# Kernel optimization log

Measured on AMD Instinct MI355X. Metric: run time of the kernel, lower is better.

## Reference

```python
import jax, jax.numpy as jnp
import numpy as np

N = 100000      # nodes
E = 1600000     # edges (avg degree 16)
IN_DIM = 64
OUT_DIM = 128
BN_EPS = 1e-5


def setup_inputs() -> dict:
    key = jax.random.key(0)
    kx, ke, kw, kb, ks = jax.random.split(key, 5)
    x = jax.random.normal(kx, (N, IN_DIM), dtype=jnp.float32)
    edge_index = jax.random.randint(ke, (2, E), 0, N, dtype=jnp.int32)
    # GCNConv linear weight (no bias inside lin; conv bias separate)
    W = jax.random.normal(kw, (IN_DIM, OUT_DIM), dtype=jnp.float32) / np.sqrt(IN_DIM)
    bias = jax.random.normal(kb, (OUT_DIM,), dtype=jnp.float32) * 0.01
    # skip projection Linear(in_dim, out_dim, bias=False)
    skip_W = jax.random.normal(ks, (IN_DIM, OUT_DIM), dtype=jnp.float32) / np.sqrt(IN_DIM)
    # BatchNorm1d affine params (training-mode batch stats used in forward)
    gamma = jnp.ones((OUT_DIM,), dtype=jnp.float32)
    beta = jnp.zeros((OUT_DIM,), dtype=jnp.float32)
    return {"x": x, "edge_index": edge_index, "W": W, "bias": bias,
            "skip_W": skip_W, "gamma": gamma, "beta": beta}


def _gcn_forward(x, edge_index, W, bias, skip_W, gamma, beta):
    n = x.shape[0]
    # GCNConv, normalize=True, add_self_loops=True (PyG defaults)
    row, col = edge_index[0], edge_index[1]
    loop = jnp.arange(n, dtype=edge_index.dtype)
    row_f = jnp.concatenate([row, loop])   # source nodes
    col_f = jnp.concatenate([col, loop])   # target nodes

    xt = x @ W                             # [N, OUT]
    deg = jax.ops.segment_sum(jnp.ones_like(col_f, dtype=xt.dtype), col_f,
                              num_segments=n)          # >= 1 due to self loops
    dinv = jax.lax.rsqrt(deg)
    norm = dinv[row_f] * dinv[col_f]                    # [E+N]
    msgs = xt[row_f] * norm[:, None]                    # gather + scale
    out = jax.ops.segment_sum(msgs, col_f, num_segments=n) + bias

    # skip-sum (in_dim != out_dim -> project)
    out = out + x @ skip_W

    # BatchNorm1d (training-mode batch statistics), affine
    mean = out.mean(axis=0)
    var = out.var(axis=0)
    out = (out - mean) * jax.lax.rsqrt(var + BN_EPS) * gamma + beta

    # ReLU; dropout p=0.0 -> identity
    return jax.nn.relu(out)


def reference(x, edge_index, W, bias, skip_W, gamma, beta):
    return _gcn_forward(x, edge_index, W, bias, skip_W, gamma, beta)
```

## Files before the change

### kernel.cpp

```cpp
#include <hip/hip_runtime.h>


typedef unsigned short ushort;
typedef __bf16 bf16x8 __attribute__((ext_vector_type(8)));
typedef float f32x4 __attribute__((ext_vector_type(4)));
typedef float f32x2 __attribute__((ext_vector_type(2)));

constexpr int N_NODES = 100000;
constexpr int N_PAD   = 100096;
constexpr int E_EDGES = 1600000;

constexpr int BUCK_SHIFT = 7;
constexpr int NBUCK   = (N_NODES + 127) / 128;
constexpr int NBUCK_P = 784;
constexpr int CHUNK   = 4096;
constexpr int NCHUNK  = (E_EDGES + CHUNK - 1) / CHUNK;
constexpr int SORT_CAP = 4096;

constexpr size_t OFF_SCALE  = 0;
constexpr size_t OFF_DINV   = 256;
constexpr size_t OFF_ROWPTR = 100352;
constexpr size_t OFF_BASE   = 200480;
constexpr size_t OFF_GHIST  = 201280;
constexpr size_t OFF_PART   = OFF_GHIST;
constexpr size_t OFF_BINNED = 507824;
constexpr size_t OFF_XB     = 2107824;
constexpr size_t OFF_U      = 5310896;
constexpr size_t OFF_PRE    = 8513968;
constexpr size_t OFF_XD8    = OFF_PRE;
constexpr size_t OFF_BT     = 14920112;

static __device__ __forceinline__ ushort f2bf(float f) {
    union { float f; unsigned u; } v; v.f = f;
    unsigned r = v.u + 0x7FFFu + ((v.u >> 16) & 1u);
    return (ushort)(r >> 16);
}
static __device__ __forceinline__ float bf2f(ushort u) {
    union { unsigned u; float f; } v; v.u = (unsigned)u << 16;
    return v.f;
}
static __device__ __forceinline__ unsigned pack_fp8x4(float a, float b, float c, float d) {
    int r = 0;
    r = __builtin_amdgcn_cvt_pk_fp8_f32(a, b, r, false);
    r = __builtin_amdgcn_cvt_pk_fp8_f32(c, d, r, true);
    return (unsigned)r;
}

__global__ void k_prep(const float* __restrict__ W, const float* __restrict__ skipW,
                       ushort* __restrict__ Bt) {
    int t = blockIdx.x * 256 + threadIdx.x;
    if (t >= 128 * 128) return;
    int k = t >> 7, n = t & 127;
    float v = (k < 64) ? W[k * 128 + n] : skipW[(k - 64) * 128 + n];
    Bt[n * 128 + k] = f2bf(v);
}

__global__ __launch_bounds__(256) void k_hist(const int* __restrict__ col,
                                              int* __restrict__ gh) {
    __shared__ int h[NBUCK_P];
    int c = blockIdx.x, t = threadIdx.x;
    for (int b = t; b < NBUCK_P; b += 256) h[b] = 0;
    __syncthreads();
    int e0 = c * CHUNK;
#pragma unroll
    for (int i = 0; i < CHUNK / 256; ++i) {
        int e = e0 + i * 256 + t;
        if (e < E_EDGES) atomicAdd(&h[col[e] >> BUCK_SHIFT], 1);
    }
    __syncthreads();
    for (int b = t; b < NBUCK_P; b += 256) gh[c * NBUCK_P + b] = h[b];
}

__global__ __launch_bounds__(512) void k_scan_buckets(int* __restrict__ gh,
                                                      int* __restrict__ base) {
    __shared__ int lds[512];
    int b = blockIdx.x, t = threadIdx.x;
    int v = (t < NCHUNK) ? gh[t * NBUCK_P + b] : 0;
    lds[t] = v;
    __syncthreads();
    int val = v;
#pragma unroll
    for (int off = 1; off < 512; off <<= 1) {
        int add = (t >= off) ? lds[t - off] : 0;
        __syncthreads();
        val += add;
        lds[t] = val;
        __syncthreads();
    }
    if (t < NCHUNK) gh[t * NBUCK_P + b] = val - v;
    if (t == 511) base[b] = val;
}

__global__ __launch_bounds__(1024) void k_scan_bases(int* __restrict__ base,
                                                     int* __restrict__ rowptr) {
    __shared__ int lds[1024];
    int t = threadIdx.x;
    int v = (t < NBUCK) ? base[t] : 0;
    lds[t] = v;
    __syncthreads();
    int val = v;
#pragma unroll
    for (int off = 1; off < 1024; off <<= 1) {
        int add = (t >= off) ? lds[t - off] : 0;
        __syncthreads();
        val += add;
        lds[t] = val;
        __syncthreads();
    }
    if (t < NBUCK) base[t] = val - v;
    if (t == 1023) {
        base[NBUCK] = val;
        rowptr[N_NODES] = val;
    }
}

__global__ __launch_bounds__(256) void k_scatter_bin(const int* __restrict__ row,
                                                     const int* __restrict__ col,
                                                     const int* __restrict__ gh,
                                                     const int* __restrict__ base,
                                                     unsigned int* __restrict__ binned) {
    __shared__ int cur[NBUCK_P];
    int c = blockIdx.x, t = threadIdx.x;
    for (int b = t; b < NBUCK_P; b += 256) {
        int bb = (b < NBUCK) ? base[b] : 0;
        cur[b] = bb + gh[c * NBUCK_P + b];
    }
    __syncthreads();
    int e0 = c * CHUNK;
#pragma unroll
    for (int i = 0; i < CHUNK / 256; ++i) {
        int e = e0 + i * 256 + t;
        if (e < E_EDGES) {
            int d = col[e];
            int s = row[e];
            int p = atomicAdd(&cur[d >> BUCK_SHIFT], 1);
            binned[p] = ((unsigned int)(d & 127) << 17) | (unsigned int)s;
        }
    }
}

__global__ __launch_bounds__(256) void k_sortbucket(unsigned int* __restrict__ binned,
                                                    const int* __restrict__ base,
                                                    int* __restrict__ rowptr,
                                                    float* __restrict__ dinv,
                                                    const float* __restrict__ x,
                                                    ushort* __restrict__ xb,
                                                    unsigned* __restrict__ xd8) {
    __shared__ unsigned int ebuf[SORT_CAP];
    __shared__ int sbuf[SORT_CAP];
    __shared__ int lcnt[128];
    __shared__ int scanb[128];
    __shared__ int lptr[128];
    __shared__ float ldinv[128];
    int b = blockIdx.x, t = threadIdx.x;
    int i0 = base[b], i1 = base[b + 1];
    int cnt = i1 - i0;
    if (cnt > SORT_CAP) cnt = SORT_CAP;
    int n0 = b << BUCK_SHIFT;
    int nn = min(128, N_NODES - n0);

    for (int k = t; k < cnt; k += 256) ebuf[k] = binned[i0 + k];
    if (t < 128) lcnt[t] = 0;
    __syncthreads();
    for (int k = t; k < cnt; k += 256) atomicAdd(&lcnt[ebuf[k] >> 17], 1);
    __syncthreads();

    int myc = (t < 128) ? lcnt[t] : 0;
    if (t < 128) scanb[t] = myc;
    __syncthreads();
    int val = myc;
#pragma unroll
    for (int off = 1; off < 128; off <<= 1) {
        int add = (t < 128 && t >= off) ? scanb[t - off] : 0;
        __syncthreads();
        if (t < 128) {
            val += add;
            scanb[t] = val;
        }
        __syncthreads();
    }
    if (t < 128) {
        int excl = val - myc;
        lptr[t] = excl;
        float dv = rsqrtf((float)myc + 1.0f);
        ldinv[t] = dv;
        if (t < nn) {
            rowptr[n0 + t] = i0 + excl;
            dinv[n0 + t] = dv;
        }
    }
    __syncthreads();
    for (int k = t; k < cnt; k += 256) {
        unsigned int e = ebuf[k];
        int j = (int)(e >> 17);
        int p = atomicAdd(&lptr[j], 1);
        sbuf[p] = (int)(e & 0x1FFFF);
    }
    __syncthreads();
    for (int k = t; k < cnt; k += 256) binned[i0 + k] = (unsigned int)sbuf[k];

#pragma unroll
    for (int it = 0; it < 8; ++it) {
        int idx = it * 256 + t;
        int nl = idx >> 4, q = idx & 15;
        int c = n0 + nl;
        ushort4 bb = {0, 0, 0, 0};
        unsigned w8 = 0;
        if (nl < nn) {
            float4 v = ((const float4*)x)[(size_t)c * 16 + q];
            bb.x = f2bf(v.x); bb.y = f2bf(v.y); bb.z = f2bf(v.z); bb.w = f2bf(v.w);
            float d = ldinv[nl];
            w8 = pack_fp8x4(v.x * d, v.y * d, v.z * d, v.w * d);
        }
        ((ushort4*)xb)[(size_t)c * 16 + q] = bb;
        xd8[(size_t)c * 16 + q] = w8;
    }
}

__global__ __launch_bounds__(256) void k_agg(const unsigned* __restrict__ xd8,
                                             const float* __restrict__ dinv,
                                             const int* __restrict__ rowptr,
                                             const unsigned int* __restrict__ csr,
                                             ushort* __restrict__ u) {
    int t = blockIdx.x * blockDim.x + threadIdx.x;
    if (t >= N_PAD * 16) return;
    int c = t >> 4;
    int q = t & 15;
    if (c >= N_NODES) {
        ushort4 z = {0, 0, 0, 0};
        ((ushort4*)u)[t] = z;
        return;
    }
    float dc = dinv[c];
    float4 acc;
    {
        unsigned w = xd8[t];
        f32x2 lo = __builtin_amdgcn_cvt_pk_f32_fp8((int)w, false);
        f32x2 hi = __builtin_amdgcn_cvt_pk_f32_fp8((int)w, true);
        acc.x = lo.x; acc.y = lo.y; acc.z = hi.x; acc.w = hi.y;
    }
    int i0 = rowptr[c], i1 = rowptr[c + 1];
    int i = i0;
    for (; i + 8 <= i1; i += 8) {
        int s[8];
#pragma unroll
        for (int k = 0; k < 8; ++k) s[k] = (int)csr[i + k];
        unsigned w[8];
#pragma unroll
        for (int k = 0; k < 8; ++k) w[k] = xd8[s[k] * 16 + q];
#pragma unroll
        for (int k = 0; k < 8; ++k) {
            f32x2 lo = __builtin_amdgcn_cvt_pk_f32_fp8((int)w[k], false);
            f32x2 hi = __builtin_amdgcn_cvt_pk_f32_fp8((int)w[k], true);
            acc.x += lo.x; acc.y += lo.y; acc.z += hi.x; acc.w += hi.y;
        }
    }
    for (; i < i1; ++i) {
        unsigned w = xd8[(int)csr[i] * 16 + q];
        f32x2 lo = __builtin_amdgcn_cvt_pk_f32_fp8((int)w, false);
        f32x2 hi = __builtin_amdgcn_cvt_pk_f32_fp8((int)w, true);
        acc.x += lo.x; acc.y += lo.y; acc.z += hi.x; acc.w += hi.y;
    }
    ushort4 o;
    o.x = f2bf(acc.x * dc); o.y = f2bf(acc.y * dc);
    o.z = f2bf(acc.z * dc); o.w = f2bf(acc.w * dc);
    ((ushort4*)u)[t] = o;
}

__global__ __launch_bounds__(256) void k_gemm(const ushort* __restrict__ u,
                                              const ushort* __restrict__ xb,
                                              const ushort* __restrict__ Bt,
                                              const float* __restrict__ bias,
                                              ushort* __restrict__ pre,
                                              float* __restrict__ partial) {
    __shared__ float sred[128];
    __shared__ float qred[128];
    int tid = threadIdx.x;
    int wave = tid >> 6, lane = tid & 63;
    int wm = wave >> 1, wn = wave & 1;
    int l15 = lane & 15, quad = lane >> 4;
    int row0 = blockIdx.x * 128 + wm * 64;
    int col0 = wn * 64;

    if (tid < 128) { sred[tid] = 0.f; qred[tid] = 0.f; }
    __syncthreads();

    bf16x8 af[4][4], bf_[4][4];
#pragma unroll
    for (int kc = 0; kc < 4; ++kc) {
        const ushort* abase = (kc < 2) ? u : xb;
        int ko = (kc & 1) * 32 + quad * 8;
#pragma unroll
        for (int im = 0; im < 4; ++im)
            af[kc][im] = *(const bf16x8*)&abase[(size_t)(row0 + im * 16 + l15) * 64 + ko];
#pragma unroll
        for (int jn = 0; jn < 4; ++jn)
            bf_[kc][jn] = *(const bf16x8*)&Bt[(size_t)(col0 + jn * 16 + l15) * 128 + kc * 32 + quad * 8];
    }

    f32x4 acc[4][4];
#pragma unroll
    for (int a = 0; a < 4; ++a)
#pragma unroll
        for (int b = 0; b < 4; ++b) acc[a][b] = (f32x4){0.f, 0.f, 0.f, 0.f};

#pragma unroll
    for (int kc = 0; kc < 4; ++kc)
#pragma unroll
        for (int im = 0; im < 4; ++im)
#pragma unroll
            for (int jn = 0; jn < 4; ++jn)
                acc[im][jn] = __builtin_amdgcn_mfma_f32_16x16x32_bf16(
                    af[kc][im], bf_[kc][jn], acc[im][jn], 0, 0, 0);

    int coln[4];
    float bi[4];
#pragma unroll
    for (int jn = 0; jn < 4; ++jn) {
        coln[jn] = col0 + jn * 16 + l15;
        bi[jn] = bias[coln[jn]];
    }
    float lsum[4] = {0.f, 0.f, 0.f, 0.f};
    float lsq[4]  = {0.f, 0.f, 0.f, 0.f};
#pragma unroll
    for (int im = 0; im < 4; ++im) {
        int rbase = row0 + im * 16 + quad * 4;
#pragma unroll
        for (int r = 0; r < 4; ++r) {
            int rowi = rbase + r;
            if (rowi < N_NODES) {
#pragma unroll
                for (int jn = 0; jn < 4; ++jn) {
                    float v = acc[im][jn][r] + bi[jn];
                    pre[(size_t)rowi * 128 + coln[jn]] = f2bf(v);
                    lsum[jn] += v;
                    lsq[jn]  += v * v;
                }
            }
        }
    }
#pragma unroll
    for (int jn = 0; jn < 4; ++jn) {
        atomicAdd(&sred[coln[jn]], lsum[jn]);
        atomicAdd(&qred[coln[jn]], lsq[jn]);
    }
    __syncthreads();
    if (tid < 128) {
        partial[(size_t)blockIdx.x * 256 + tid]       = sred[tid];
        partial[(size_t)blockIdx.x * 256 + 128 + tid] = qred[tid];
    }
}

__global__ __launch_bounds__(256) void k_reduce(const float* __restrict__ partial,
                                                const float* __restrict__ gamma,
                                                const float* __restrict__ beta,
                                                float* __restrict__ scaleshift) {
    __shared__ float ls[256], lq[256];
    int j = blockIdx.x;
    int t = threadIdx.x;
    float s = 0.f, q = 0.f;
    for (int p = t; p < NBUCK; p += 256) {
        s += partial[(size_t)p * 256 + j];
        q += partial[(size_t)p * 256 + 128 + j];
    }
    ls[t] = s; lq[t] = q;
    __syncthreads();
#pragma unroll
    for (int off = 128; off > 0; off >>= 1) {
        if (t < off) { ls[t] += ls[t + off]; lq[t] += lq[t + off]; }
        __syncthreads();
    }
    if (t == 0) {
        float mean = ls[0] * (1.0f / N_NODES);
        float var  = lq[0] * (1.0f / N_NODES) - mean * mean;
        float sc   = gamma[j] * rsqrtf(var + 1e-5f);
        scaleshift[j]       = sc;
        scaleshift[128 + j] = beta[j] - mean * sc;
    }
}

__global__ void k_apply(const ushort* __restrict__ pre, float* __restrict__ out,
                        const float* __restrict__ scaleshift) {
    int t = blockIdx.x * blockDim.x + threadIdx.x;
    if (t >= N_NODES * 32) return;
    int j4 = t & 31;
    ushort4 p = ((const ushort4*)pre)[t];
    float4 sc = ((const float4*)scaleshift)[j4];
    float4 sh = ((const float4*)(scaleshift + 128))[j4];
    float4 v;
    v.x = fmaxf(fmaf(bf2f(p.x), sc.x, sh.x), 0.f);
    v.y = fmaxf(fmaf(bf2f(p.y), sc.y, sh.y), 0.f);
    v.z = fmaxf(fmaf(bf2f(p.z), sc.z, sh.z), 0.f);
    v.w = fmaxf(fmaf(bf2f(p.w), sc.w, sh.w), 0.f);
    ((float4*)out)[t] = v;
}

extern "C" void kernel_launch(void* const* d_in, const int* in_sizes, int n_in,
                              void* d_out, int out_size, void* d_ws, size_t ws_size,
                              hipStream_t stream) {
    const float* x      = (const float*)d_in[0];
    const int*   eidx   = (const int*)d_in[1];
    const float* W      = (const float*)d_in[2];
    const float* bias   = (const float*)d_in[3];
    const float* skipW  = (const float*)d_in[4];
    const float* gamma  = (const float*)d_in[5];
    const float* beta   = (const float*)d_in[6];
    float* out = (float*)d_out;
    float* ws  = (float*)d_ws;

    const int* row = eidx;
    const int* col = eidx + E_EDGES;

    float* scaleshift = ws + OFF_SCALE;
    float* dinv       = ws + OFF_DINV;
    int*   rowptr     = (int*)(ws + OFF_ROWPTR);
    int*   base       = (int*)(ws + OFF_BASE);
    int*   gh         = (int*)(ws + OFF_GHIST);
    float* partial    = ws + OFF_PART;
    unsigned int* binned = (unsigned int*)(ws + OFF_BINNED);
    ushort* xb        = (ushort*)(ws + OFF_XB);
    ushort* u         = (ushort*)(ws + OFF_U);
    unsigned* xd8     = (unsigned*)(ws + OFF_XD8);
    ushort* pre       = (ushort*)(ws + OFF_PRE);
    ushort* Bt        = (ushort*)(ws + OFF_BT);

    k_prep<<<64, 256, 0, stream>>>(W, skipW, Bt);
    k_hist<<<NCHUNK, 256, 0, stream>>>(col, gh);
    k_scan_buckets<<<NBUCK, 512, 0, stream>>>(gh, base);
    k_scan_bases<<<1, 1024, 0, stream>>>(base, rowptr);
    k_scatter_bin<<<NCHUNK, 256, 0, stream>>>(row, col, gh, base, binned);
    k_sortbucket<<<NBUCK, 256, 0, stream>>>(binned, base, rowptr, dinv, x, xb, xd8);
    k_agg<<<(N_PAD * 16 + 255) / 256, 256, 0, stream>>>(xd8, dinv, rowptr, binned, u);
    k_gemm<<<NBUCK, 256, 0, stream>>>(u, xb, Bt, bias, pre, partial);
    k_reduce<<<128, 256, 0, stream>>>(partial, gamma, beta, scaleshift);
    k_apply<<<(N_NODES * 32 + 255) / 256, 256, 0, stream>>>(pre, out, scaleshift);
}
```

Baseline: 230.0 us.

## Merge prep into hist, fuse base scan via last-block, vectorize edge loads

Folds the weight transpose/convert kernel into the histogram kernel as extra blocks. It also removes the separate single-block base-scan kernel by having the last-finishing bucket-scan block, detected with an atomic counter, do the final scan. Edge index loads in hist and scatter are vectorized to int4, and the per-bucket 128-entry scan uses wavefront shuffles instead of LDS barriers. The aim is fewer kernel launches and less sync overhead, at the cost of an extra memset and reliance on atomic release/acquire ordering.

```diff
diff --git a/kernel.cpp b/kernel.cpp
--- a/kernel.cpp
+++ b/kernel.cpp
@@ -21,6 +21,7 @@
 constexpr size_t OFF_DINV   = 256;
 constexpr size_t OFF_ROWPTR = 100352;
 constexpr size_t OFF_BASE   = 200480;
+constexpr size_t OFF_DONE   = 201272;
 constexpr size_t OFF_GHIST  = 201280;
 constexpr size_t OFF_PART   = OFF_GHIST;
 constexpr size_t OFF_BINNED = 507824;
@@ -46,34 +47,51 @@
     return (unsigned)r;
 }
 
-__global__ void k_prep(const float* __restrict__ W, const float* __restrict__ skipW,
-                       ushort* __restrict__ Bt) {
-    int t = blockIdx.x * 256 + threadIdx.x;
-    if (t >= 128 * 128) return;
-    int k = t >> 7, n = t & 127;
-    float v = (k < 64) ? W[k * 128 + n] : skipW[(k - 64) * 128 + n];
-    Bt[n * 128 + k] = f2bf(v);
-}
-
 __global__ __launch_bounds__(256) void k_hist(const int* __restrict__ col,
-                                              int* __restrict__ gh) {
+                                              int* __restrict__ gh,
+                                              const float* __restrict__ W,
+                                              const float* __restrict__ skipW,
+                                              ushort* __restrict__ Bt) {
+    int c = blockIdx.x, t = threadIdx.x;
+    if (c >= NCHUNK) {
+        int idx = (c - NCHUNK) * 256 + t;
+        int k = idx >> 7, n = idx & 127;
+        float v = (k < 64) ? W[k * 128 + n] : skipW[(k - 64) * 128 + n];
+        Bt[n * 128 + k] = f2bf(v);
+        return;
+    }
     __shared__ int h[NBUCK_P];
-    int c = blockIdx.x, t = threadIdx.x;
     for (int b = t; b < NBUCK_P; b += 256) h[b] = 0;
     __syncthreads();
-    int e0 = c * CHUNK;
-#pragma unroll
-    for (int i = 0; i < CHUNK / 256; ++i) {
-        int e = e0 + i * 256 + t;
-        if (e < E_EDGES) atomicAdd(&h[col[e] >> BUCK_SHIFT], 1);
+    const int4* col4 = (const int4*)col;
+    int g0 = c * (CHUNK / 4);
+#pragma unroll
+    for (int i = 0; i < CHUNK / 1024; ++i) {
+        int g4 = g0 + i * 256 + t;
+        if (g4 * 4 + 3 < E_EDGES) {
+            int4 cc = col4[g4];
+            atomicAdd(&h[cc.x >> BUCK_SHIFT], 1);
+            atomicAdd(&h[cc.y >> BUCK_SHIFT], 1);
+            atomicAdd(&h[cc.z >> BUCK_SHIFT], 1);
+            atomicAdd(&h[cc.w >> BUCK_SHIFT], 1);
+        } else {
+#pragma unroll
+            for (int j = 0; j < 4; ++j) {
+                int e = g4 * 4 + j;
+                if (e < E_EDGES) atomicAdd(&h[col[e] >> BUCK_SHIFT], 1);
+            }
+        }
     }
     __syncthreads();
     for (int b = t; b < NBUCK_P; b += 256) gh[c * NBUCK_P + b] = h[b];
 }
 
 __global__ __launch_bounds__(512) void k_scan_buckets(int* __restrict__ gh,
-                                                      int* __restrict__ base) {
-    __shared__ int lds[512];
+                                                      int* __restrict__ base,
+                                                      int* __restrict__ rowptr,
+                                                      int* __restrict__ done) {
+    __shared__ int lds[1024];
+    __shared__ int lastflag;
     int b = blockIdx.x, t = threadIdx.x;
     int v = (t < NCHUNK) ? gh[t * NBUCK_P + b] : 0;
     lds[t] = v;
@@ -88,29 +106,35 @@
         __syncthreads();
     }
     if (t < NCHUNK) gh[t * NBUCK_P + b] = val - v;
-    if (t == 511) base[b] = val;
-}
-
-__global__ __launch_bounds__(1024) void k_scan_bases(int* __restrict__ base,
-                                                     int* __restrict__ rowptr) {
-    __shared__ int lds[1024];
-    int t = threadIdx.x;
-    int v = (t < NBUCK) ? base[t] : 0;
-    lds[t] = v;
-    __syncthreads();
-    int val = v;
+    if (t == 511) {
+        __hip_atomic_store(&base[b], val, __ATOMIC_RELEASE, __HIP_MEMORY_SCOPE_AGENT);
+        int old = __hip_atomic_fetch_add(done, 1, __ATOMIC_ACQ_REL, __HIP_MEMORY_SCOPE_AGENT);
+        lastflag = (old == NBUCK - 1) ? 1 : 0;
+    }
+    __syncthreads();
+    if (!lastflag) return;
+
+    int v0 = (t < NBUCK) ? __hip_atomic_load(&base[t], __ATOMIC_ACQUIRE, __HIP_MEMORY_SCOPE_AGENT) : 0;
+    int v1 = (512 + t < NBUCK) ? __hip_atomic_load(&base[512 + t], __ATOMIC_ACQUIRE, __HIP_MEMORY_SCOPE_AGENT) : 0;
+    __syncthreads();
+    lds[t] = v0;
+    lds[512 + t] = v1;
+    __syncthreads();
 #pragma unroll
     for (int off = 1; off < 1024; off <<= 1) {
-        int add = (t >= off) ? lds[t - off] : 0;
+        int a0 = (t >= off) ? lds[t - off] : 0;
+        int a1 = (512 + t >= off) ? lds[512 + t - off] : 0;
         __syncthreads();
-        val += add;
-        lds[t] = val;
+        lds[t] += a0;
+        lds[512 + t] += a1;
         __syncthreads();
     }
-    if (t < NBUCK) base[t] = val - v;
-    if (t == 1023) {
-        base[NBUCK] = val;
-        rowptr[N_NODES] = val;
+    if (t < NBUCK) base[t] = lds[t] - v0;
+    if (512 + t < NBUCK) base[512 + t] = lds[512 + t] - v1;
+    if (t == 511) {
+        int total = lds[1023];
+        base[NBUCK] = total;
+        rowptr[N_NODES] = total;
     }
 }
 
@@ -126,15 +150,34 @@
         cur[b] = bb + gh[c * NBUCK_P + b];
     }
     __syncthreads();
-    int e0 = c * CHUNK;
-#pragma unroll
-    for (int i = 0; i < CHUNK / 256; ++i) {
-        int e = e0 + i * 256 + t;
-        if (e < E_EDGES) {
-            int d = col[e];
-            int s = row[e];
-            int p = atomicAdd(&cur[d >> BUCK_SHIFT], 1);
-            binned[p] = ((unsigned int)(d & 127) << 17) | (unsigned int)s;
+    const int4* col4 = (const int4*)col;
+    const int4* row4 = (const int4*)row;
+    int g0 = c * (CHUNK / 4);
+#pragma unroll
+    for (int i = 0; i < CHUNK / 1024; ++i) {
+        int g4 = g0 + i * 256 + t;
+        if (g4 * 4 + 3 < E_EDGES) {
+            int4 cc = col4[g4];
+            int4 rr = row4[g4];
+            int p;
+            p = atomicAdd(&cur[cc.x >> BUCK_SHIFT], 1);
+            binned[p] = ((unsigned)(cc.x & 127) << 17) | (unsigned)rr.x;
+            p = atomicAdd(&cur[cc.y >> BUCK_SHIFT], 1);
+            binned[p] = ((unsigned)(cc.y & 127) << 17) | (unsigned)rr.y;
+            p = atomicAdd(&cur[cc.z >> BUCK_SHIFT], 1);
+            binned[p] = ((unsigned)(cc.z & 127) << 17) | (unsigned)rr.z;
+            p = atomicAdd(&cur[cc.w >> BUCK_SHIFT], 1);
+            binned[p] = ((unsigned)(cc.w & 127) << 17) | (unsigned)rr.w;
+        } else {
+#pragma unroll
+            for (int j = 0; j < 4; ++j) {
+                int e = g4 * 4 + j;
+                if (e < E_EDGES) {
+                    int d = col[e], s = row[e];
+                    int p = atomicAdd(&cur[d >> BUCK_SHIFT], 1);
+                    binned[p] = ((unsigned)(d & 127) << 17) | (unsigned)s;
+                }
+            }
         }
     }
 }
@@ -149,9 +192,9 @@
     __shared__ unsigned int ebuf[SORT_CAP];
     __shared__ int sbuf[SORT_CAP];
     __shared__ int lcnt[128];
-    __shared__ int scanb[128];
     __shared__ int lptr[128];
     __shared__ float ldinv[128];
+    __shared__ int wsum[2];
     int b = blockIdx.x, t = threadIdx.x;
     int i0 = base[b], i1 = base[b + 1];
     int cnt = i1 - i0;
@@ -165,21 +208,20 @@
     for (int k = t; k < cnt; k += 256) atomicAdd(&lcnt[ebuf[k] >> 17], 1);
     __syncthreads();
 
-    int myc = (t < 128) ? lcnt[t] : 0;
-    if (t < 128) scanb[t] = myc;
-    __syncthreads();
-    int val = myc;
-#pragma unroll
-    for (int off = 1; off < 128; off <<= 1) {
-        int add = (t < 128 && t >= off) ? scanb[t - off] : 0;
-        __syncthreads();
-        if (t < 128) {
-            val += add;
-            scanb[t] = val;
-        }
-        __syncthreads();
-    }
+    int myc = 0, val = 0;
     if (t < 128) {
+        myc = lcnt[t];
+        val = myc;
+#pragma unroll
+        for (int d = 1; d < 64; d <<= 1) {
+            int o = __shfl_up(val, d);
+            if ((t & 63) >= d) val += o;
+        }
+        if ((t & 63) == 63) wsum[t >> 6] = val;
+    }
+    __syncthreads();
+    if (t < 128) {
+        if (t >= 64) val += wsum[0];
         int excl = val - myc;
         lptr[t] = excl;
         float dv = rsqrtf((float)myc + 1.0f);
@@ -415,6 +457,7 @@
     float* dinv       = ws + OFF_DINV;
     int*   rowptr     = (int*)(ws + OFF_ROWPTR);
     int*   base       = (int*)(ws + OFF_BASE);
+    int*   done       = (int*)(ws + OFF_DONE);
     int*   gh         = (int*)(ws + OFF_GHIST);
     float* partial    = ws + OFF_PART;
     unsigned int* binned = (unsigned int*)(ws + OFF_BINNED);
@@ -424,10 +467,10 @@
     ushort* pre       = (ushort*)(ws + OFF_PRE);
     ushort* Bt        = (ushort*)(ws + OFF_BT);
 
-    k_prep<<<64, 256, 0, stream>>>(W, skipW, Bt);
-    k_hist<<<NCHUNK, 256, 0, stream>>>(col, gh);
-    k_scan_buckets<<<NBUCK, 512, 0, stream>>>(gh, base);
-    k_scan_bases<<<1, 1024, 0, stream>>>(base, rowptr);
+    hipMemsetAsync(done, 0, 8, stream);
+
+    k_hist<<<NCHUNK + 64, 256, 0, stream>>>(col, gh, W, skipW, Bt);
+    k_scan_buckets<<<NBUCK, 512, 0, stream>>>(gh, base, rowptr, done);
     k_scatter_bin<<<NCHUNK, 256, 0, stream>>>(row, col, gh, base, binned);
     k_sortbucket<<<NBUCK, 256, 0, stream>>>(binned, base, rowptr, dinv, x, xb, xd8);
     k_agg<<<(N_PAD * 16 + 255) / 256, 256, 0, stream>>>(xd8, dinv, rowptr, binned, u);
```

New measurement: 263.5 us. 14.5% more time.
